# Kernel tuning notes

Measured on AMD Instinct MI355X. Metric: run time of the kernel, lower is better.

The kernel has to match this reference:

```python
import jax, jax.numpy as jnp
import numpy as np
import math

B, S, D, H = 2, 2048, 1024, 16
DK = D // H
SCALE = math.sqrt(DK)
NEG_BIG = -1e9


def setup_inputs() -> dict:
    key = jax.random.key(0)
    ks = jax.random.split(key, 7)
    x = jax.random.normal(ks[0], (B, S, D), dtype=jnp.float32)
    # additive causal mask: 0 on/below diagonal, -inf above
    causal = jnp.triu(jnp.ones((S, S), dtype=bool), k=1)
    mask = jnp.where(causal, -jnp.inf, 0.0).astype(jnp.float32)
    key_padding_mask = jax.random.bernoulli(ks[1], 0.1, (B, S))
    init = 1.0 / math.sqrt(D)
    Wq = jax.random.normal(ks[2], (D, D), dtype=jnp.float32) * init
    Wk = jax.random.normal(ks[3], (D, D), dtype=jnp.float32) * init
    Wv = jax.random.normal(ks[4], (D, D), dtype=jnp.float32) * init
    Wo = jax.random.normal(ks[5], (D, D), dtype=jnp.float32) * init
    bo = jnp.zeros((D,), dtype=jnp.float32)
    return {"x": x, "mask": mask, "key_padding_mask": key_padding_mask,
            "Wq": Wq, "Wk": Wk, "Wv": Wv, "Wo": Wo, "bo": bo}


def reference(x, mask, key_padding_mask, Wq, Wk, Wv, Wo, bo):
    b, s, d = x.shape
    # project and split heads -> [B,H,S,Dk]
    def heads(W):
        return jnp.einsum('bsd,de->bse', x, W).reshape(b, s, H, DK).transpose(0, 2, 1, 3)
    Q, K, V = heads(Wq), heads(Wk), heads(Wv)
    scores = jnp.einsum('bhqd,bhkd->bhqk', Q, K) / SCALE          # [B,H,S,S]
    scores = scores + mask[None, None]                            # additive attn mask
    scores = jnp.where(key_padding_mask[:, None, None, :], -jnp.inf, scores)
    # rows whose max is -inf (fully masked) get all scores set to -1e9
    max_scores = jnp.max(scores, axis=-1, keepdims=True)
    scores = jnp.where(jnp.isinf(max_scores), NEG_BIG, scores)
    attn = jax.nn.softmax(scores, axis=-1)
    attn = jnp.where(jnp.isnan(attn), 0.0, attn)
    # dropout is identity in eval mode
    ctx = jnp.einsum('bhqk,bhkd->bhqd', attn, V)                  # [B,H,S,Dk]
    ctx = ctx.transpose(0, 2, 1, 3).reshape(b, s, d)
    return jnp.einsum('bsd,de->bse', ctx, Wo) + bo
```

## Files before the change

kernel.cpp:

```cpp
#include <hip/hip_runtime.h>
#include <stdint.h>

#define NB 2
#define NS 2048
#define ND 1024
#define NH 16
#define NDK 64

typedef __attribute__((ext_vector_type(8))) short s8v;
typedef __attribute__((ext_vector_type(4))) float f4v;
typedef __attribute__((ext_vector_type(4))) unsigned short us4v;
typedef __attribute__((ext_vector_type(8))) unsigned short us8v;
typedef __attribute__((ext_vector_type(2))) uint32_t u2v;

__device__ __forceinline__ unsigned short f2bf(float f) {
  uint32_t u = __builtin_bit_cast(uint32_t, f);
  u = (u + 0x7fffu + ((u >> 16) & 1u)) >> 16;
  return (unsigned short)u;
}
__device__ __forceinline__ float bf2f(unsigned short h) {
  uint32_t u = ((uint32_t)h) << 16;
  return __builtin_bit_cast(float, u);
}
__device__ __forceinline__ uint32_t cvtpk(float lo, float hi) {
  uint32_t r;
  asm("v_cvt_pk_bf16_f32 %0, %1, %2" : "=v"(r) : "v"(lo), "v"(hi));
  return r;
}

__device__ __forceinline__ void gload16(const void* g, void* l) {
  __builtin_amdgcn_global_load_lds(
      (const __attribute__((address_space(1))) void*)g,
      (__attribute__((address_space(3))) void*)l, 16, 0, 0);
}

__global__ void k_convert_x(const float* __restrict__ x, unsigned short* __restrict__ xbf) {
  int i = (blockIdx.x * 256 + threadIdx.x) * 4;
  float4 v = *(const float4*)(x + i);
  us4v o;
  o[0] = f2bf(v.x); o[1] = f2bf(v.y); o[2] = f2bf(v.z); o[3] = f2bf(v.w);
  *(us4v*)(xbf + i) = o;
}

__global__ void k_transpose_w(const float* __restrict__ Wq, const float* __restrict__ Wk,
                              const float* __restrict__ Wv, const float* __restrict__ Wo,
                              unsigned short* __restrict__ wt_qkv, unsigned short* __restrict__ wt_o) {
  __shared__ float tls[64][65];
  int bid = blockIdx.x;
  int mat = bid >> 8;
  int tile = bid & 255;
  int tk = tile >> 4, tn = tile & 15;
  const float* W = (mat == 0) ? Wq : (mat == 1) ? Wk : (mat == 2) ? Wv : Wo;
  int t = threadIdx.x;
  int lr = t >> 2;
  int lc0 = (t & 3) * 16;
  const float* src = W + (size_t)(tk * 64 + lr) * 1024 + tn * 64 + lc0;
#pragma unroll
  for (int j = 0; j < 16; j += 4) {
    float4 v = *(const float4*)(src + j);
    tls[lr][lc0 + j + 0] = v.x; tls[lr][lc0 + j + 1] = v.y;
    tls[lr][lc0 + j + 2] = v.z; tls[lr][lc0 + j + 3] = v.w;
  }
  __syncthreads();
  float scale = (mat == 0) ? 0.18033688f : 1.0f;
  int nr = t >> 2, kc0 = (t & 3) * 16;
  unsigned short* dst = ((mat < 3) ? (wt_qkv + (size_t)(mat * 1024 + tn * 64 + nr) * 1024)
                                   : (wt_o + (size_t)(tn * 64 + nr) * 1024)) + tk * 64 + kc0;
  us8v o0, o1;
#pragma unroll
  for (int j = 0; j < 8; j++) o0[j] = f2bf(tls[kc0 + j][nr] * scale);
#pragma unroll
  for (int j = 0; j < 8; j++) o1[j] = f2bf(tls[kc0 + 8 + j][nr] * scale);
  *(us8v*)(dst) = o0;
  *(us8v*)(dst + 8) = o1;
}

__global__ __launch_bounds__(256) void k_gemm0(const unsigned short* __restrict__ A,
                                               const unsigned short* __restrict__ Bt,
                                               unsigned short* __restrict__ qklin,
                                               unsigned short* __restrict__ vt) {
  __shared__ unsigned short smem[6 * 128 * 32];
#define SA(b_) (smem + (b_)*4096)
#define SB(b_) (smem + 12288 + (b_)*4096)
  const int K = 1024;
  const int NT = K / 32;
  int bid = blockIdx.x;
  int xcd = bid & 7, local = bid >> 3;
  int m0 = (xcd * 4 + (local & 3)) * 128;
  int n0 = (local >> 2) * 128;
  int tid = threadIdx.x, lane = tid & 63, w = tid >> 6;
  int wm = w >> 1, wn = w & 1;
  int g = lane >> 4, c0 = lane & 15;
  int rrel = lane >> 2;
  int gran = lane & 3;
  int rsw = (rrel >> 1) & 3;
  int csw = (c0 >> 1) & 3;
  f4v acc[4][4];
#pragma unroll
  for (int mi = 0; mi < 4; mi++)
#pragma unroll
    for (int ni = 0; ni < 4; ni++) acc[mi][ni] = (f4v){0.f, 0.f, 0.f, 0.f};

#define STAGE(kt_, buf_)                                                        \
  do {                                                                          \
    int koff = (kt_)*32;                                                        \
    _Pragma("unroll") for (int i = 0; i < 2; i++) {                             \
      int r = 32 * w + 16 * i + rrel;                                           \
      gload16(A + (size_t)(m0 + r) * K + koff + 8 * (gran ^ rsw),               \
              (void*)(SA(buf_) + (32 * w + 16 * i) * 32));                      \
      gload16(Bt + (size_t)(n0 + r) * K + koff + 8 * (gran ^ rsw),              \
              (void*)(SB(buf_) + (32 * w + 16 * i) * 32));                      \
    }                                                                           \
  } while (0)

  STAGE(0, 0);
  STAGE(1, 1);
  asm volatile("s_waitcnt vmcnt(4)" ::: "memory");
  __builtin_amdgcn_s_barrier();
  __builtin_amdgcn_sched_barrier(0);

  for (int kt = 0; kt < NT; ++kt) {
    int cur = kt % 3;
    if (kt + 2 < NT) STAGE(kt + 2, (kt + 2) % 3);
    s8v af[4], bfr[4];
#pragma unroll
    for (int mi = 0; mi < 4; mi++) {
      int row = 64 * wm + 16 * mi + c0;
      af[mi] = *(const s8v*)(SA(cur) + row * 32 + 8 * (g ^ csw));
    }
#pragma unroll
    for (int ni = 0; ni < 4; ni++) {
      int row = 64 * wn + 16 * ni + c0;
      bfr[ni] = *(const s8v*)(SB(cur) + row * 32 + 8 * (g ^ csw));
    }
#pragma unroll
    for (int mi = 0; mi < 4; mi++)
#pragma unroll
      for (int ni = 0; ni < 4; ni++)
        acc[mi][ni] = __builtin_amdgcn_mfma_f32_16x16x32_bf16(af[mi], bfr[ni], acc[mi][ni], 0, 0, 0);
    if (kt + 1 < NT) {
      if (kt + 2 < NT) {
        asm volatile("s_waitcnt vmcnt(4)" ::: "memory");
      } else {
        asm volatile("s_waitcnt vmcnt(0)" ::: "memory");
      }
      __builtin_amdgcn_s_barrier();
      __builtin_amdgcn_sched_barrier(0);
    }
  }
#undef STAGE

  if (n0 < 2048) {
#pragma unroll
    for (int mi = 0; mi < 4; mi++)
#pragma unroll
      for (int ni = 0; ni < 4; ni++)
#pragma unroll
        for (int r = 0; r < 4; r++) {
          int m = m0 + 64 * wm + 16 * mi + 4 * g + r;
          int n = n0 + 64 * wn + 16 * ni + c0;
          qklin[(size_t)m * 2048 + n] = f2bf(acc[mi][ni][r]);
        }
  } else {
    const int PAD = 132;
    unsigned short* tl = smem;
    __syncthreads();
#pragma unroll
    for (int mi = 0; mi < 4; mi++)
#pragma unroll
      for (int ni = 0; ni < 4; ni++) {
        int nloc = 64 * wn + 16 * ni + c0;
        int m4 = 64 * wm + 16 * mi + 4 * g;
        us4v pk;
#pragma unroll
        for (int r = 0; r < 4; r++) pk[r] = f2bf(acc[mi][ni][r]);
        *(us4v*)(tl + nloc * PAD + m4) = pk;
      }
    __syncthreads();
    int row = tid >> 1, half = tid & 1;
    int n = n0 + row;
    int hh = (n - 2048) >> 6, dk = n & 63;
    int bb = m0 >> 11;
    int s0 = (m0 & 2047) + 64 * half;
    unsigned short* dstp = vt + (size_t)((bb * 16 + hh) * 64 + dk) * 2048 + s0;
    const unsigned short* srcp = tl + row * PAD + 64 * half;
#pragma unroll
    for (int j = 0; j < 8; j++) {
      us4v lo = *(const us4v*)(srcp + 8 * j);
      us4v hi = *(const us4v*)(srcp + 8 * j + 4);
      us8v v8;
      v8[0] = lo[0]; v8[1] = lo[1]; v8[2] = lo[2]; v8[3] = lo[3];
      v8[4] = hi[0]; v8[5] = hi[1]; v8[6] = hi[2]; v8[7] = hi[3];
      *(us8v*)(dstp + 8 * j) = v8;
    }
  }
#undef SA
#undef SB
}

__global__ __launch_bounds__(256) void k_gemm1(const unsigned short* __restrict__ A,
                                               const unsigned short* __restrict__ Bt,
                                               const float* __restrict__ bias,
                                               float* __restrict__ out) {
  __shared__ unsigned short lds_a[2][64 * 32];
  __shared__ unsigned short lds_b[2][64 * 32];
  const int K = 1024;
  const int NT = K / 32;
  int bid = blockIdx.x;
  int xcd = bid & 7, local = bid >> 3;
  int m0 = (xcd * 8 + (local & 7)) * 64;
  int n0 = (local >> 3) * 64;
  int tid = threadIdx.x, lane = tid & 63, w = tid >> 6;
  int wm = w >> 1, wn = w & 1;
  int g = lane >> 4, c0 = lane & 15;
  int rrel = lane >> 2;
  int gran = lane & 3;
  int rsw = (rrel >> 1) & 3;
  int csw = (c0 >> 1) & 3;
  f4v acc[2][2];
#pragma unroll
  for (int mi = 0; mi < 2; mi++)
#pragma unroll
    for (int ni = 0; ni < 2; ni++) acc[mi][ni] = (f4v){0.f, 0.f, 0.f, 0.f};

#define STAGE1(kt_, buf_)                                                       \
  do {                                                                          \
    int koff = (kt_)*32;                                                        \
    int r = 16 * w + rrel;                                                      \
    gload16(A + (size_t)(m0 + r) * K + koff + 8 * (gran ^ rsw),                 \
            (void*)(lds_a[buf_] + (16 * w) * 32));                              \
    gload16(Bt + (size_t)(n0 + r) * K + koff + 8 * (gran ^ rsw),                \
            (void*)(lds_b[buf_] + (16 * w) * 32));                              \
  } while (0)

  STAGE1(0, 0);
  __syncthreads();

  for (int kt = 0; kt < NT; ++kt) {
    int cur = kt & 1;
    if (kt + 1 < NT) STAGE1(kt + 1, cur ^ 1);
    s8v af[2], bfr[2];
#pragma unroll
    for (int mi = 0; mi < 2; mi++) {
      int row = 32 * wm + 16 * mi + c0;
      af[mi] = *(const s8v*)(lds_a[cur] + row * 32 + 8 * (g ^ csw));
    }
#pragma unroll
    for (int ni = 0; ni < 2; ni++) {
      int row = 32 * wn + 16 * ni + c0;
      bfr[ni] = *(const s8v*)(lds_b[cur] + row * 32 + 8 * (g ^ csw));
    }
#pragma unroll
    for (int mi = 0; mi < 2; mi++)
#pragma unroll
      for (int ni = 0; ni < 2; ni++)
        acc[mi][ni] = __builtin_amdgcn_mfma_f32_16x16x32_bf16(af[mi], bfr[ni], acc[mi][ni], 0, 0, 0);
    __syncthreads();
  }
#undef STAGE1

#pragma unroll
  for (int mi = 0; mi < 2; mi++)
#pragma unroll
    for (int ni = 0; ni < 2; ni++)
#pragma unroll
      for (int r = 0; r < 4; r++) {
        int m = m0 + 32 * wm + 16 * mi + 4 * g + r;
        int n = n0 + 32 * wn + 16 * ni + c0;
        out[(size_t)m * 1024 + n] = acc[mi][ni][r] + bias[n];
      }
}

__global__ void k_vmean(const unsigned short* __restrict__ vt, float* __restrict__ vmean) {
  int row = blockIdx.x * 4 + (threadIdx.x >> 6);
  int lane = threadIdx.x & 63;
  const unsigned short* p = vt + (size_t)row * 2048 + lane * 32;
  float s = 0.f;
#pragma unroll
  for (int j = 0; j < 32; j += 8) {
    us8v v = *(const us8v*)(p + j);
#pragma unroll
    for (int e = 0; e < 8; e++) s += bf2f(v[e]);
  }
#pragma unroll
  for (int m = 1; m < 64; m <<= 1) s += __shfl_xor(s, m);
  if (lane == 0) vmean[row] = s * (1.0f / 2048.0f);
}

__global__ __launch_bounds__(256) void k_attn(const unsigned short* __restrict__ qklin,
                                              const unsigned short* __restrict__ vt,
                                              const int* __restrict__ kpm,
                                              const float* __restrict__ vmean,
                                              unsigned short* __restrict__ ctx) {
  __shared__ unsigned short lds_k[2][64 * 64];
  __shared__ unsigned short lds_v[2][64 * 64];
  __shared__ unsigned short p_lds[4][16 * 64];
  int wg = blockIdx.x;
  int w5 = wg >> 5, bh = wg & 31;
  int qt = (w5 < 8) ? 31 - w5 : (w5 < 16) ? w5 - 8 : (w5 < 24) ? 39 - w5 : w5 - 16;
  int b = bh >> 4, h = bh & 15;
  int tid = threadIdx.x, lane = tid & 63, w = tid >> 6;
  int g = lane >> 4, c0 = lane & 15;
  int q0 = qt * 64 + w * 16;
  unsigned short* pl = p_lds[w];
  int rrel = lane >> 3, gran = lane & 7;

  const unsigned short* ksrc0 = qklin + (size_t)(b * NS) * 2048 + 1024 + h * 64;
  const unsigned short* vsrc0 = vt + (size_t)(bh * 64) * 2048;

  const unsigned short* qbase = qklin + (size_t)(b * NS + q0 + c0) * 2048 + h * 64 + 8 * g;
  s8v qf0 = *(const s8v*)(qbase);
  s8v qf1 = *(const s8v*)(qbase + 32);

  f4v cacc[4];
#pragma unroll
  for (int d = 0; d < 4; d++) cacc[d] = (f4v){0.f, 0.f, 0.f, 0.f};
  float m_s = -1e30f, l_s = 0.f;
  int qrow = q0 + c0;

#define STAGEKV(it_, buf_)                                                      \
  do {                                                                          \
    int kb_ = (it_)*64;                                                         \
    _Pragma("unroll") for (int i = 0; i < 2; i++) {                             \
      int r = 16 * w + 8 * i + rrel;                                            \
      gload16(ksrc0 + (size_t)(kb_ + r) * 2048 + 8 * (gran ^ rrel),             \
              (void*)(lds_k[buf_] + (16 * w + 8 * i) * 64));                    \
      gload16(vsrc0 + (size_t)r * 2048 + kb_ + 8 * (gran ^ rrel),               \
              (void*)(lds_v[buf_] + (16 * w + 8 * i) * 64));                    \
    }                                                                           \
  } while (0)

  STAGEKV(0, 0);
  int kp_cur = kpm[b * NS + lane];

  int nkt = qt + 1;
  for (int it = 0; it < nkt; ++it) {
    int kb = it * 64;
    int cur = it & 1;
    int kp_next = 0;
    if (it + 1 < nkt) {
      STAGEKV(it + 1, cur ^ 1);
      kp_next = kpm[b * NS + (it + 1) * 64 + lane];
      asm volatile("s_waitcnt vmcnt(5)" ::: "memory");
    } else {
      asm volatile("s_waitcnt vmcnt(0)" ::: "memory");
    }
    __builtin_amdgcn_s_barrier();
    __builtin_amdgcn_sched_barrier(0);
    uint64_t padmask = __ballot(kp_cur != 0);
    f4v sacc[4];
#pragma unroll
    for (int t = 0; t < 4; t++) {
      int row = 16 * t + c0;
      s8v kf0 = *(const s8v*)(lds_k[cur] + row * 64 + 8 * (g ^ (c0 & 7)));
      s8v kf1 = *(const s8v*)(lds_k[cur] + row * 64 + 8 * ((4 + g) ^ (c0 & 7)));
      f4v z = (f4v){0.f, 0.f, 0.f, 0.f};
      z = __builtin_amdgcn_mfma_f32_16x16x32_bf16(kf0, qf0, z, 0, 0, 0);
      z = __builtin_amdgcn_mfma_f32_16x16x32_bf16(kf1, qf1, z, 0, 0, 0);
      sacc[t] = z;
    }
    int thr = qrow - kb;
    uint64_t cmask = (thr >= 63) ? ~0ull : ((2ull << thr) - 1ull);
    uint64_t valid = cmask & ~padmask;
    uint32_t vlo = (uint32_t)valid, vhi = (uint32_t)(valid >> 32);
    float p[4][4];
    float mx = -1e30f;
#pragma unroll
    for (int t = 0; t < 4; t++) {
      uint32_t half = (t & 2) ? vhi : vlo;
      uint32_t nib = (half >> (16 * (t & 1) + 4 * g)) & 0xFu;
#pragma unroll
      for (int r = 0; r < 4; r++) {
        float s = sacc[t][r];
        s = ((nib >> r) & 1u) ? s : -1e30f;
        p[t][r] = s;
      }
      mx = fmaxf(mx, fmaxf(fmaxf(p[t][0], p[t][1]), fmaxf(p[t][2], p[t][3])));
    }
    mx = fmaxf(mx, __shfl_xor(mx, 16));
    mx = fmaxf(mx, __shfl_xor(mx, 32));
    if (!__all(mx <= m_s + 11.0f)) {
      float mnew = fmaxf(m_s, mx);
      float a = __builtin_exp2f(m_s - mnew);
      m_s = mnew;
      l_s *= a;
      int ybase = 20 * g;
#pragma unroll
      for (int r = 0; r < 4; r++) {
        float ar = __shfl(a, ybase + r);
#pragma unroll
        for (int d = 0; d < 4; d++) cacc[d][r] *= ar;
      }
    }
    float rs = 0.f;
#pragma unroll
    for (int t = 0; t < 4; t++)
#pragma unroll
      for (int r = 0; r < 4; r++) {
        float e = __builtin_exp2f(p[t][r] - m_s);
        p[t][r] = e;
        rs += e;
      }
    rs += __shfl_xor(rs, 16);
    rs += __shfl_xor(rs, 32);
    rs = (m_s > -1e29f) ? rs : 0.f;
    l_s += rs;
#pragma unroll
    for (int t = 0; t < 4; t++) {
      u2v pk;
      pk[0] = cvtpk(p[t][0], p[t][1]);
      pk[1] = cvtpk(p[t][2], p[t][3]);
      int gr = (2 * t + (g >> 1)) ^ (c0 & 7);
      *(u2v*)((char*)pl + c0 * 128 + gr * 16 + 8 * (g & 1)) = pk;
    }
    asm volatile("s_waitcnt lgkmcnt(0)" ::: "memory");
    __builtin_amdgcn_sched_barrier(0);
#pragma unroll
    for (int c = 0; c < 2; c++) {
      int off = c0 * 128 + 16 * g + 64 * c;
      off ^= (c0 & 7) << 4;
      s8v pf = *(const s8v*)((const char*)pl + off);
#pragma unroll
      for (int d = 0; d < 4; d++) {
        int row = 16 * d + c0;
        s8v vf = *(const s8v*)(lds_v[cur] + row * 64 + 8 * ((4 * c + g) ^ (c0 & 7)));
        cacc[d] = __builtin_amdgcn_mfma_f32_16x16x32_bf16(pf, vf, cacc[d], 0, 0, 0);
      }
    }
    __builtin_amdgcn_s_barrier();
    __builtin_amdgcn_sched_barrier(0);
    kp_cur = kp_next;
  }
#undef STAGEKV
  float lq[4];
  {
    int ybase = 20 * g;
#pragma unroll
    for (int r = 0; r < 4; r++) lq[r] = __shfl(l_s, ybase + r);
  }
#pragma unroll
  for (int d = 0; d < 4; d++)
#pragma unroll
    for (int r = 0; r < 4; r++) {
      int q = q0 + 4 * g + r;
      float l = lq[r];
      float v = (l > 0.f) ? cacc[d][r] / l : vmean[bh * 64 + 16 * d + c0];
      ctx[(size_t)(b * NS + q) * ND + h * 64 + 16 * d + c0] = f2bf(v);
    }
}

extern "C" void kernel_launch(void* const* d_in, const int* in_sizes, int n_in,
                              void* d_out, int out_size, void* d_ws, size_t ws_size,
                              hipStream_t stream) {
  const float* x  = (const float*)d_in[0];
  const int* kpm  = (const int*)d_in[2];
  const float* Wq = (const float*)d_in[3];
  const float* Wk = (const float*)d_in[4];
  const float* Wv = (const float*)d_in[5];
  const float* Wo = (const float*)d_in[6];
  const float* bo = (const float*)d_in[7];

  char* ws = (char*)d_ws;
  unsigned short* xbf   = (unsigned short*)(ws);
  unsigned short* wtqkv = (unsigned short*)(ws + 8u * 1024 * 1024);
  unsigned short* wto   = (unsigned short*)(ws + 14u * 1024 * 1024);
  unsigned short* vt    = (unsigned short*)(ws + 16u * 1024 * 1024);
  float* vmean          = (float*)(ws + 24u * 1024 * 1024);
  unsigned short* ctx   = xbf;
  unsigned short* qklin = (unsigned short*)d_out;

  k_convert_x<<<4096, 256, 0, stream>>>(x, xbf);
  k_transpose_w<<<1024, 256, 0, stream>>>(Wq, Wk, Wv, Wo, wtqkv, wto);
  k_gemm0<<<768, 256, 0, stream>>>(xbf, wtqkv, qklin, vt);
  k_vmean<<<512, 256, 0, stream>>>(vt, vmean);
  k_attn<<<1024, 256, 0, stream>>>(qklin, vt, kpm, vmean, ctx);
  k_gemm1<<<1024, 256, 0, stream>>>(ctx, wto, bo, (float*)d_out);
}
```

Baseline: 133.4 us.

## Fuse prep kernels, fold V-mean into GEMM epilogue, compute row sums via MFMA

Merges the x-conversion and weight-transpose kernels into a single launch. It removes the separate V-mean kernel by accumulating per-column sums with atomics in the V-projection epilogue, which needs a memset before it. In attention, the softmax row-sum is now accumulated by an extra MFMA against a ones vector instead of VALU adds and cross-lane shuffles, and the max reduction uses v_max3. Together these cut launch count and VALU work in the inner loop, at the cost of extra MFMA issue, fp32 atomics, and sums taken over bf16-rounded P values.

Measured after the change: 129.1 us. 1.03x faster.

```diff
diff --git a/kernel.cpp b/kernel.cpp
--- a/kernel.cpp
+++ b/kernel.cpp
@@ -12,6 +12,7 @@
 typedef __attribute__((ext_vector_type(4))) unsigned short us4v;
 typedef __attribute__((ext_vector_type(8))) unsigned short us8v;
 typedef __attribute__((ext_vector_type(2))) uint32_t u2v;
+typedef __attribute__((ext_vector_type(4))) uint32_t u4v;
 
 __device__ __forceinline__ unsigned short f2bf(float f) {
   uint32_t u = __builtin_bit_cast(uint32_t, f);
@@ -27,6 +28,11 @@
   asm("v_cvt_pk_bf16_f32 %0, %1, %2" : "=v"(r) : "v"(lo), "v"(hi));
   return r;
 }
+__device__ __forceinline__ float max3f(float a, float b, float c) {
+  float r;
+  asm("v_max3_f32 %0, %1, %2, %3" : "=v"(r) : "v"(a), "v"(b), "v"(c));
+  return r;
+}
 
 __device__ __forceinline__ void gload16(const void* g, void* l) {
   __builtin_amdgcn_global_load_lds(
@@ -34,19 +40,20 @@
       (__attribute__((address_space(3))) void*)l, 16, 0, 0);
 }
 
-__global__ void k_convert_x(const float* __restrict__ x, unsigned short* __restrict__ xbf) {
-  int i = (blockIdx.x * 256 + threadIdx.x) * 4;
-  float4 v = *(const float4*)(x + i);
-  us4v o;
-  o[0] = f2bf(v.x); o[1] = f2bf(v.y); o[2] = f2bf(v.z); o[3] = f2bf(v.w);
-  *(us4v*)(xbf + i) = o;
-}
-
-__global__ void k_transpose_w(const float* __restrict__ Wq, const float* __restrict__ Wk,
-                              const float* __restrict__ Wv, const float* __restrict__ Wo,
-                              unsigned short* __restrict__ wt_qkv, unsigned short* __restrict__ wt_o) {
+__global__ void k_prep(const float* __restrict__ x, unsigned short* __restrict__ xbf,
+                       const float* __restrict__ Wq, const float* __restrict__ Wk,
+                       const float* __restrict__ Wv, const float* __restrict__ Wo,
+                       unsigned short* __restrict__ wt_qkv, unsigned short* __restrict__ wt_o) {
   __shared__ float tls[64][65];
-  int bid = blockIdx.x;
+  if (blockIdx.x < 4096) {
+    int i = (blockIdx.x * 256 + threadIdx.x) * 4;
+    float4 v = *(const float4*)(x + i);
+    us4v o;
+    o[0] = f2bf(v.x); o[1] = f2bf(v.y); o[2] = f2bf(v.z); o[3] = f2bf(v.w);
+    *(us4v*)(xbf + i) = o;
+    return;
+  }
+  int bid = blockIdx.x - 4096;
   int mat = bid >> 8;
   int tile = bid & 255;
   int tk = tile >> 4, tn = tile & 15;
@@ -78,7 +85,8 @@
 __global__ __launch_bounds__(256) void k_gemm0(const unsigned short* __restrict__ A,
                                                const unsigned short* __restrict__ Bt,
                                                unsigned short* __restrict__ qklin,
-                                               unsigned short* __restrict__ vt) {
+                                               unsigned short* __restrict__ vt,
+                                               float* __restrict__ vmean) {
   __shared__ unsigned short smem[6 * 128 * 32];
 #define SA(b_) (smem + (b_)*4096)
 #define SB(b_) (smem + 12288 + (b_)*4096)
@@ -162,6 +170,22 @@
           qklin[(size_t)m * 2048 + n] = f2bf(acc[mi][ni][r]);
         }
   } else {
+    int bb = m0 >> 11;
+#pragma unroll
+    for (int ni = 0; ni < 4; ni++) {
+      float s = 0.f;
+#pragma unroll
+      for (int mi = 0; mi < 4; mi++)
+#pragma unroll
+        for (int r = 0; r < 4; r++) s += acc[mi][ni][r];
+      s += __shfl_xor(s, 16);
+      s += __shfl_xor(s, 32);
+      if ((lane >> 4) == 0) {
+        int n = n0 + 64 * wn + 16 * ni + c0;
+        int hh = (n - 2048) >> 6, dk = n & 63;
+        atomicAdd(vmean + (bb * 16 + hh) * 64 + dk, s);
+      }
+    }
     const int PAD = 132;
     unsigned short* tl = smem;
     __syncthreads();
@@ -180,7 +204,6 @@
     int row = tid >> 1, half = tid & 1;
     int n = n0 + row;
     int hh = (n - 2048) >> 6, dk = n & 63;
-    int bb = m0 >> 11;
     int s0 = (m0 & 2047) + 64 * half;
     unsigned short* dstp = vt + (size_t)((bb * 16 + hh) * 64 + dk) * 2048 + s0;
     const unsigned short* srcp = tl + row * PAD + 64 * half;
@@ -271,22 +294,6 @@
       }
 }
 
-__global__ void k_vmean(const unsigned short* __restrict__ vt, float* __restrict__ vmean) {
-  int row = blockIdx.x * 4 + (threadIdx.x >> 6);
-  int lane = threadIdx.x & 63;
-  const unsigned short* p = vt + (size_t)row * 2048 + lane * 32;
-  float s = 0.f;
-#pragma unroll
-  for (int j = 0; j < 32; j += 8) {
-    us8v v = *(const us8v*)(p + j);
-#pragma unroll
-    for (int e = 0; e < 8; e++) s += bf2f(v[e]);
-  }
-#pragma unroll
-  for (int m = 1; m < 64; m <<= 1) s += __shfl_xor(s, m);
-  if (lane == 0) vmean[row] = s * (1.0f / 2048.0f);
-}
-
 __global__ __launch_bounds__(256) void k_attn(const unsigned short* __restrict__ qklin,
                                               const unsigned short* __restrict__ vt,
                                               const int* __restrict__ kpm,
@@ -312,10 +319,15 @@
   s8v qf0 = *(const s8v*)(qbase);
   s8v qf1 = *(const s8v*)(qbase + 32);
 
+  const uint32_t one2 = 0x3F803F80u;
+  u4v onesw = {one2, one2, one2, one2};
+  s8v ones = __builtin_bit_cast(s8v, onesw);
+
   f4v cacc[4];
 #pragma unroll
   for (int d = 0; d < 4; d++) cacc[d] = (f4v){0.f, 0.f, 0.f, 0.f};
-  float m_s = -1e30f, l_s = 0.f;
+  f4v lsum = (f4v){0.f, 0.f, 0.f, 0.f};
+  float m_s = -1e30f;
   int qrow = q0 + c0;
 
 #define STAGEKV(it_, buf_)                                                      \
@@ -364,7 +376,6 @@
     uint64_t valid = cmask & ~padmask;
     uint32_t vlo = (uint32_t)valid, vhi = (uint32_t)(valid >> 32);
     float p[4][4];
-    float mx = -1e30f;
 #pragma unroll
     for (int t = 0; t < 4; t++) {
       uint32_t half = (t & 2) ? vhi : vlo;
@@ -375,36 +386,32 @@
         s = ((nib >> r) & 1u) ? s : -1e30f;
         p[t][r] = s;
       }
-      mx = fmaxf(mx, fmaxf(fmaxf(p[t][0], p[t][1]), fmaxf(p[t][2], p[t][3])));
-    }
+    }
+    float a0 = max3f(p[0][0], p[0][1], p[0][2]);
+    float a1 = max3f(p[0][3], p[1][0], p[1][1]);
+    float a2 = max3f(p[1][2], p[1][3], p[2][0]);
+    float a3 = max3f(p[2][1], p[2][2], p[2][3]);
+    float a4 = max3f(p[3][0], p[3][1], p[3][2]);
+    float mx = fmaxf(max3f(a0, a1, a2), max3f(a3, a4, p[3][3]));
     mx = fmaxf(mx, __shfl_xor(mx, 16));
     mx = fmaxf(mx, __shfl_xor(mx, 32));
     if (!__all(mx <= m_s + 11.0f)) {
       float mnew = fmaxf(m_s, mx);
       float a = __builtin_exp2f(m_s - mnew);
       m_s = mnew;
-      l_s *= a;
       int ybase = 20 * g;
 #pragma unroll
       for (int r = 0; r < 4; r++) {
         float ar = __shfl(a, ybase + r);
+        lsum[r] *= ar;
 #pragma unroll
         for (int d = 0; d < 4; d++) cacc[d][r] *= ar;
       }
     }
-    float rs = 0.f;
 #pragma unroll
     for (int t = 0; t < 4; t++)
 #pragma unroll
-      for (int r = 0; r < 4; r++) {
-        float e = __builtin_exp2f(p[t][r] - m_s);
-        p[t][r] = e;
-        rs += e;
-      }
-    rs += __shfl_xor(rs, 16);
-    rs += __shfl_xor(rs, 32);
-    rs = (m_s > -1e29f) ? rs : 0.f;
-    l_s += rs;
+      for (int r = 0; r < 4; r++) p[t][r] = __builtin_exp2f(p[t][r] - m_s);
 #pragma unroll
     for (int t = 0; t < 4; t++) {
       u2v pk;
@@ -426,25 +433,27 @@
         s8v vf = *(const s8v*)(lds_v[cur] + row * 64 + 8 * ((4 * c + g) ^ (c0 & 7)));
         cacc[d] = __builtin_amdgcn_mfma_f32_16x16x32_bf16(pf, vf, cacc[d], 0, 0, 0);
       }
+      lsum = __builtin_amdgcn_mfma_f32_16x16x32_bf16(pf, ones, lsum, 0, 0, 0);
     }
     __builtin_amdgcn_s_barrier();
     __builtin_amdgcn_sched_barrier(0);
     kp_cur = kp_next;
   }
 #undef STAGEKV
-  float lq[4];
+  float mq[4];
   {
     int ybase = 20 * g;
 #pragma unroll
-    for (int r = 0; r < 4; r++) lq[r] = __shfl(l_s, ybase + r);
+    for (int r = 0; r < 4; r++) mq[r] = __shfl(m_s, ybase + r);
   }
 #pragma unroll
   for (int d = 0; d < 4; d++)
 #pragma unroll
     for (int r = 0; r < 4; r++) {
       int q = q0 + 4 * g + r;
-      float l = lq[r];
-      float v = (l > 0.f) ? cacc[d][r] / l : vmean[bh * 64 + 16 * d + c0];
+      float l = (mq[r] > -1e29f) ? lsum[r] : 0.f;
+      float v = (l > 0.f) ? cacc[d][r] / l
+                          : vmean[bh * 64 + 16 * d + c0] * (1.0f / 2048.0f);
       ctx[(size_t)(b * NS + q) * ND + h * 64 + 16 * d + c0] = f2bf(v);
     }
 }
@@ -469,10 +478,9 @@
   unsigned short* ctx   = xbf;
   unsigned short* qklin = (unsigned short*)d_out;
 
-  k_convert_x<<<4096, 256, 0, stream>>>(x, xbf);
-  k_transpose_w<<<1024, 256, 0, stream>>>(Wq, Wk, Wv, Wo, wtqkv, wto);
-  k_gemm0<<<768, 256, 0, stream>>>(xbf, wtqkv, qklin, vt);
-  k_vmean<<<512, 256, 0, stream>>>(vt, vmean);
+  hipMemsetAsync(vmean, 0, 2048 * sizeof(float), stream);
+  k_prep<<<5120, 256, 0, stream>>>(x, xbf, Wq, Wk, Wv, Wo, wtqkv, wto);
+  k_gemm0<<<768, 256, 0, stream>>>(xbf, wtqkv, qklin, vt, vmean);
   k_attn<<<1024, 256, 0, stream>>>(qklin, vt, kpm, vmean, ctx);
   k_gemm1<<<1024, 256, 0, stream>>>(ctx, wto, bo, (float*)d_out);
 }
```
